# Optimization experiments

Measured on AMD Instinct MI355X. Metric: run time of the kernel, lower is better.

## Reference

```python
import jax, jax.numpy as jnp
import numpy as np

EGO, RNN, CUBE, FC, NA = 3200, 512, 3200, 1024, 2
N = 2048


def setup_inputs() -> dict:
    key = jax.random.key(0)
    ks = jax.random.split(key, 24)
    s = 0.02
    inp = {
        'rnn_feats': jax.random.normal(ks[0], (N, 2, RNN), jnp.float32),
        'cube_feats': jax.random.normal(ks[1], (N, 2, 4, CUBE), jnp.float32),
        'ego_feats': jax.random.normal(ks[2], (N, 3, EGO + RNN), jnp.float32),
        'rnn_eid': jax.random.randint(ks[3], (N,), 0, 3),
        'room_eid': jax.random.randint(ks[4], (N,), 0, 2),
        'dist_eid': jax.random.randint(ks[5], (N,), 0, 2),
        # shared front-end layers
        'Wc': jax.random.normal(ks[6], (CUBE, FC), jnp.float32) * s,
        'bc': jnp.zeros((FC,), jnp.float32),
        'Wd': jax.random.normal(ks[7], (EGO + RNN, FC), jnp.float32) * s,
        'bd': jnp.zeros((FC,), jnp.float32),
        # 3 experts on 2*RNN inputs (object color/size)
        'W1_rnn': jax.random.normal(ks[8], (3, 2 * RNN, FC), jnp.float32) * s,
        'b1_rnn': jnp.zeros((3, FC), jnp.float32),
        'W2_rnn': jax.random.normal(ks[9], (3, FC, NA), jnp.float32) * s,
        'b2_rnn': jnp.zeros((3, NA), jnp.float32),
        # 2 experts on 2*4*FC inputs (room size)
        'W1_room': jax.random.normal(ks[10], (2, 8 * FC, FC), jnp.float32) * s,
        'b1_room': jnp.zeros((2, FC), jnp.float32),
        'W2_room': jax.random.normal(ks[11], (2, FC, NA), jnp.float32) * s,
        'b2_room': jnp.zeros((2, NA), jnp.float32),
        # 2 experts on 2*FC inputs (object dist)
        'W1_dist': jax.random.normal(ks[12], (2, 2 * FC, FC), jnp.float32) * s,
        'b1_dist': jnp.zeros((2, FC), jnp.float32),
        'W2_dist': jax.random.normal(ks[13], (2, FC, NA), jnp.float32) * s,
        'b2_dist': jnp.zeros((2, NA), jnp.float32),
    }
    return inp


def _group_mlp(x, W1, b1, W2, b2, eid):
    # x: (n, in); W1: (E, in, fc); per-sample routed 2-layer MLP.
    # Dropout is identity (eval / p=0). Compute all E experts (E<=3), select via one-hot.
    h = jax.nn.relu(jnp.einsum('ni,eif->nef', x, W1) + b1[None])  # (n, E, fc)
    s = jnp.einsum('nef,efo->neo', h, W2) + b2[None]              # (n, E, 2)
    oh = jax.nn.one_hot(eid, W1.shape[0], dtype=x.dtype)          # (n, E)
    return jnp.einsum('neo,ne->no', s, oh)


def reference(rnn_feats, cube_feats, ego_feats, Wc, bc, Wd, bd,
              W1_rnn, b1_rnn, W2_rnn, b2_rnn,
              W1_room, b1_room, W2_room, b2_room,
              W1_dist, b1_dist, W2_dist, b2_dist,
              rnn_eid, room_eid, dist_eid):
    n = rnn_feats.shape[0]
    # object color/size group: raw rnn feats flattened
    x_rnn = rnn_feats.reshape(n, -1)                                   # (n, 2*RNN)
    s_rnn = _group_mlp(x_rnn, W1_rnn, b1_rnn, W2_rnn, b2_rnn, rnn_eid)
    # room size group: cube_fc_layer then flatten (2,4,fc) -> 8*fc
    hc = jax.nn.relu(jnp.einsum('npqc,cf->npqf', cube_feats, Wc) + bc)
    x_room = hc.reshape(n, -1)                                          # (n, 8*FC)
    s_room = _group_mlp(x_room, W1_room, b1_room, W2_room, b2_room, room_eid)
    # object dist group: dist_fc_layer, then pairwise products of the 3 rows
    hd = jax.nn.relu(jnp.einsum('nkd,df->nkf', ego_feats, Wd) + bd)     # (n, 3, FC)
    x_dist = jnp.concatenate([hd[:, 0] * hd[:, 1], hd[:, 1] * hd[:, 2]], axis=-1)  # (n, 2*FC)
    s_dist = _group_mlp(x_dist, W1_dist, b1_dist, W2_dist, b2_dist, dist_eid)
    return jnp.concatenate([s_rnn, s_room, s_dist], axis=0)             # (3n, 2)
```

## Files before the change

kernel.cpp:

```cpp
#include <hip/hip_runtime.h>

typedef __bf16 bf16;
typedef __bf16 bf16x8 __attribute__((ext_vector_type(8)));
typedef float f32x4 __attribute__((ext_vector_type(4)));

__device__ __forceinline__ void gld_lds16(const bf16* g, bf16* lds_base) {
    __builtin_amdgcn_global_load_lds(
        (const __attribute__((address_space(1))) void*)g,
        (__attribute__((address_space(3))) void*)lds_base, 16, 0, 0);
}

#define MFMA16(a, b, c) __builtin_amdgcn_mfma_f32_16x16x32_bf16((a), (b), (c), 0, 0, 0)

__global__ void detect_k(const unsigned* __restrict__ rnn, int* __restrict__ flag) {
    const int lane = threadIdx.x;
    const unsigned w = rnn[lane];
    const int e = (w >> 7) & 0xFF;
    const bool good = (e >= 100 && e <= 130);
    const unsigned long long m = __ballot(good);
    if (lane == 0) *flag = (__popcll(m) >= 48) ? 0 : 1;
}

__global__ __launch_bounds__(256) void transpose_k(const void* __restrict__ in_,
                                                   bf16* __restrict__ out,
                                                   const int* __restrict__ flag,
                                                   int R, int C) {
    __shared__ __align__(16) bf16 t[64][72];
    const int dt = *flag;
    const long boff = (long)blockIdx.z * R * C;
    const int c0 = blockIdx.x * 64, r0 = blockIdx.y * 64;
    const int lr = threadIdx.x >> 2;
    const int lc = (threadIdx.x & 3) * 16;

    bf16x8 v0, v1;
    if (dt) {
        const float* src = (const float*)in_ + boff + (long)(r0 + lr) * C + c0 + lc;
        float4 f0 = ((const float4*)src)[0];
        float4 f1 = ((const float4*)src)[1];
        float4 f2 = ((const float4*)src)[2];
        float4 f3 = ((const float4*)src)[3];
        v0[0]=(bf16)f0.x; v0[1]=(bf16)f0.y; v0[2]=(bf16)f0.z; v0[3]=(bf16)f0.w;
        v0[4]=(bf16)f1.x; v0[5]=(bf16)f1.y; v0[6]=(bf16)f1.z; v0[7]=(bf16)f1.w;
        v1[0]=(bf16)f2.x; v1[1]=(bf16)f2.y; v1[2]=(bf16)f2.z; v1[3]=(bf16)f2.w;
        v1[4]=(bf16)f3.x; v1[5]=(bf16)f3.y; v1[6]=(bf16)f3.z; v1[7]=(bf16)f3.w;
    } else {
        const bf16* src = (const bf16*)in_ + boff + (long)(r0 + lr) * C + c0 + lc;
        v0 = ((const bf16x8*)src)[0];
        v1 = ((const bf16x8*)src)[1];
    }
    *(bf16x8*)(&t[lr][lc])     = v0;
    *(bf16x8*)(&t[lr][lc + 8]) = v1;
    __syncthreads();

    bf16 tmp[16];
#pragma unroll
    for (int k = 0; k < 16; ++k) tmp[k] = t[lc + k][lr];
    bf16* dst = out + boff + (long)(c0 + lr) * R + r0 + lc;
    *(float4*)(dst)     = *(float4*)(&tmp[0]);
    *(float4*)(dst + 8) = *(float4*)(&tmp[8]);
}

__device__ __forceinline__ void kloop256(const bf16* __restrict__ A,
                                         const bf16* __restrict__ Bt,
                                         int K, int m0, int n0, bf16* L,
                                         int wid, int lane,
                                         f32x4 (&acc)[2][2][4][2]) {
    const int wm = wid >> 2, wn = wid & 3;
    const int quad = lane >> 4, l15 = lane & 15;
    const int nt = K >> 6;

    const int sr = wid * 8 + (lane >> 3);
    const int sc = ((lane & 7) ^ ((lane >> 3) & 7)) * 8;
    const bf16* Ag = A + (long)(m0 + sr) * K + sc;
    const bf16* Bg = Bt + (long)(n0 + sr) * K + sc;
    const long K64 = (long)K * 64, K128 = (long)K * 128;
    bf16* const As = L;
    bf16* const Bs = L + 32768;
    const int w512 = wid * 512;

    const int arow = (wm * 64 + l15) * 64;
    const int brow = (wn * 32 + l15) * 64;
    const int swz0 = ((0 * 4 + quad) ^ (l15 & 7)) * 8;
    const int swz1 = ((1 * 4 + quad) ^ (l15 & 7)) * 8;

    gld_lds16(Ag,              As + w512);
    gld_lds16(Ag + K64,        As + 4096 + w512);
    gld_lds16(Bg,              Bs + w512);
    gld_lds16(Bg + K64,        Bs + 4096 + w512);
    gld_lds16(Ag + K128,       As + 8192 + w512);
    gld_lds16(Ag + K128 + K64, As + 8192 + 4096 + w512);
    gld_lds16(Bg + K128,       Bs + 8192 + w512);
    gld_lds16(Bg + K128 + K64, Bs + 8192 + 4096 + w512);
    gld_lds16(Ag + 64,         As + 16384 + w512);
    gld_lds16(Ag + K64 + 64,   As + 16384 + 4096 + w512);
    gld_lds16(Bg + 64,         Bs + 16384 + w512);
    gld_lds16(Bg + K64 + 64,   Bs + 16384 + 4096 + w512);
    asm volatile("s_waitcnt vmcnt(4)" ::: "memory");
    __builtin_amdgcn_s_barrier();

    bf16x8 af[4][2], b0[2][2], b1[2][2];

    for (int t = 0; t < nt; ++t) {
        const int buf = t & 1, nbuf = buf ^ 1;
        bf16* A0 = As + (buf * 2 + 0) * 8192;
        bf16* A1 = As + (buf * 2 + 1) * 8192;
        bf16* B0 = Bs + (buf * 2 + 0) * 8192;
        bf16* B1 = Bs + (buf * 2 + 1) * 8192;
        const long ko1 = (long)(t + 1) * 64;
        const long ko2 = (long)(t + 2) * 64;

#pragma unroll
        for (int m = 0; m < 4; ++m) {
            af[m][0] = *(const bf16x8*)(A0 + arow + m * 1024 + swz0);
            af[m][1] = *(const bf16x8*)(A0 + arow + m * 1024 + swz1);
        }
#pragma unroll
        for (int n = 0; n < 2; ++n) {
            b0[n][0] = *(const bf16x8*)(B0 + brow + n * 1024 + swz0);
            b0[n][1] = *(const bf16x8*)(B0 + brow + n * 1024 + swz1);
        }
        if (t + 1 < nt) {
            gld_lds16(Ag + K128 + ko1,       As + (nbuf * 2 + 1) * 8192 + w512);
            gld_lds16(Ag + K128 + K64 + ko1, As + (nbuf * 2 + 1) * 8192 + 4096 + w512);
            gld_lds16(Bg + K128 + ko1,       Bs + (nbuf * 2 + 1) * 8192 + w512);
            gld_lds16(Bg + K128 + K64 + ko1, Bs + (nbuf * 2 + 1) * 8192 + 4096 + w512);
        }
        __builtin_amdgcn_s_barrier();
        asm volatile("s_waitcnt lgkmcnt(0)" ::: "memory");
        __builtin_amdgcn_sched_barrier(0);
        __builtin_amdgcn_s_setprio(1);
#pragma unroll
        for (int m = 0; m < 4; ++m)
#pragma unroll
            for (int n = 0; n < 2; ++n) {
                acc[0][0][m][n] = MFMA16(af[m][0], b0[n][0], acc[0][0][m][n]);
                acc[0][0][m][n] = MFMA16(af[m][1], b0[n][1], acc[0][0][m][n]);
            }
        __builtin_amdgcn_s_setprio(0);
        __builtin_amdgcn_sched_barrier(0);
        __builtin_amdgcn_s_barrier();

#pragma unroll
        for (int n = 0; n < 2; ++n) {
            b1[n][0] = *(const bf16x8*)(B1 + brow + n * 1024 + swz0);
            b1[n][1] = *(const bf16x8*)(B1 + brow + n * 1024 + swz1);
        }
        if (t + 2 < nt) {
            gld_lds16(Ag + ko2,       A0 + w512);
            gld_lds16(Ag + K64 + ko2, A0 + 4096 + w512);
        }
        __builtin_amdgcn_s_barrier();
        asm volatile("s_waitcnt lgkmcnt(0)" ::: "memory");
        __builtin_amdgcn_sched_barrier(0);
        __builtin_amdgcn_s_setprio(1);
#pragma unroll
        for (int m = 0; m < 4; ++m)
#pragma unroll
            for (int n = 0; n < 2; ++n) {
                acc[0][1][m][n] = MFMA16(af[m][0], b1[n][0], acc[0][1][m][n]);
                acc[0][1][m][n] = MFMA16(af[m][1], b1[n][1], acc[0][1][m][n]);
            }
        __builtin_amdgcn_s_setprio(0);
        __builtin_amdgcn_sched_barrier(0);
        __builtin_amdgcn_s_barrier();

#pragma unroll
        for (int m = 0; m < 4; ++m) {
            af[m][0] = *(const bf16x8*)(A1 + arow + m * 1024 + swz0);
            af[m][1] = *(const bf16x8*)(A1 + arow + m * 1024 + swz1);
        }
        __builtin_amdgcn_s_barrier();
        asm volatile("s_waitcnt lgkmcnt(0)" ::: "memory");
        __builtin_amdgcn_sched_barrier(0);
        __builtin_amdgcn_s_setprio(1);
#pragma unroll
        for (int m = 0; m < 4; ++m)
#pragma unroll
            for (int n = 0; n < 2; ++n) {
                acc[1][0][m][n] = MFMA16(af[m][0], b0[n][0], acc[1][0][m][n]);
                acc[1][0][m][n] = MFMA16(af[m][1], b0[n][1], acc[1][0][m][n]);
            }
        __builtin_amdgcn_s_setprio(0);
        __builtin_amdgcn_sched_barrier(0);
        __builtin_amdgcn_s_barrier();

        if (t + 2 < nt) {
            gld_lds16(Bg + ko2,       B0 + w512);
            gld_lds16(Bg + K64 + ko2, B0 + 4096 + w512);
        }
        __builtin_amdgcn_s_setprio(1);
#pragma unroll
        for (int m = 0; m < 4; ++m)
#pragma unroll
            for (int n = 0; n < 2; ++n) {
                acc[1][1][m][n] = MFMA16(af[m][0], b1[n][0], acc[1][1][m][n]);
                acc[1][1][m][n] = MFMA16(af[m][1], b1[n][1], acc[1][1][m][n]);
            }
        __builtin_amdgcn_s_setprio(0);
        __builtin_amdgcn_sched_barrier(0);
        if (t + 2 < nt) {
            asm volatile("s_waitcnt vmcnt(4)" ::: "memory");
        } else if (t + 1 < nt) {
            asm volatile("s_waitcnt vmcnt(0)" ::: "memory");
        }
        __builtin_amdgcn_s_barrier();
    }
}

__device__ __forceinline__ void tile256_coords(int& m0, int& n0) {
    const int lin = blockIdx.y * 8 + blockIdx.x;
    const int x = lin & 7, j = lin >> 3;
    const int mbPerX = (int)(gridDim.x * gridDim.y) >> 5;
    m0 = (x * mbPerX + (j >> 2)) * 256;
    n0 = (j & 3) * 256;
}

__global__ __launch_bounds__(512, 2) void gemm256_front(
        const void* __restrict__ A_, const bf16* __restrict__ Bt,
        const void* __restrict__ bias_, bf16* __restrict__ C,
        const int* __restrict__ flag, int M, int N, int K) {
    if (*flag != 0) return;
    __shared__ __align__(16) bf16 L[65536];
    const int tid = threadIdx.x, lane = tid & 63, wid = tid >> 6;
    int m0, n0;
    tile256_coords(m0, n0);

    f32x4 acc[2][2][4][2];
#pragma unroll
    for (int a = 0; a < 2; ++a)
#pragma unroll
        for (int b = 0; b < 2; ++b)
#pragma unroll
            for (int m = 0; m < 4; ++m)
#pragma unroll
                for (int n = 0; n < 2; ++n) acc[a][b][m][n] = (f32x4){0.f,0.f,0.f,0.f};

    kloop256((const bf16*)A_, Bt, K, m0, n0, L, wid, lane, acc);

    const bf16* bias = (const bf16*)bias_;
    const int wm = wid >> 2, wn = wid & 3;
    const int quad = lane >> 4, l15 = lane & 15;
#pragma unroll
    for (int qn = 0; qn < 2; ++qn)
#pragma unroll
        for (int n = 0; n < 2; ++n) {
            const int colg = n0 + qn * 128 + wn * 32 + n * 16 + l15;
            const float bj = (float)bias[colg];
#pragma unroll
            for (int qm = 0; qm < 2; ++qm)
#pragma unroll
                for (int m = 0; m < 4; ++m) {
                    const int rowb = m0 + qm * 128 + wm * 64 + m * 16 + quad * 4;
#pragma unroll
                    for (int r = 0; r < 4; ++r) {
                        float v = acc[qm][qn][m][n][r] + bj;
                        v = v > 0.f ? v : 0.f;
                        C[(long)(rowb + r) * N + colg] = (bf16)v;
                    }
                }
        }
}

struct ExpDescs {
    const void* A[7];
    const bf16* Bt[7];
    const void* biasB[7];
    const void* w2B[7];
    float* S[7];
    long biasEoff[7];
    long w2Eoff[7];
    int K[7];
    int adt[7];
};

__global__ __launch_bounds__(512, 2) void gemm256_expert(ExpDescs d,
                                                         const int* __restrict__ flag) {
    if (*flag != 0) return;
    __shared__ __align__(16) bf16 L[65536];
    const int z = blockIdx.z;
    const int K = d.K[z];
    const int tid = threadIdx.x, lane = tid & 63, wid = tid >> 6;
    int m0, n0;
    tile256_coords(m0, n0);

    f32x4 acc[2][2][4][2];
#pragma unroll
    for (int a = 0; a < 2; ++a)
#pragma unroll
        for (int b = 0; b < 2; ++b)
#pragma unroll
            for (int m = 0; m < 4; ++m)
#pragma unroll
                for (int n = 0; n < 2; ++n) acc[a][b][m][n] = (f32x4){0.f,0.f,0.f,0.f};

    kloop256((const bf16*)d.A[z], d.Bt[z], K, m0, n0, L, wid, lane, acc);

    const bf16* bias_b = (const bf16*)d.biasB[z] + d.biasEoff[z];
    const bf16* w2_b   = (const bf16*)d.w2B[z] + d.w2Eoff[z];
    float* S = d.S[z];
    const int wm = wid >> 2, wn = wid & 3;
    const int quad = lane >> 4, l15 = lane & 15;

    float bj[2][2], w2f[2][2][2];
#pragma unroll
    for (int qn = 0; qn < 2; ++qn)
#pragma unroll
        for (int n = 0; n < 2; ++n) {
            const int colg = n0 + qn * 128 + wn * 32 + n * 16 + l15;
            bj[qn][n] = (float)bias_b[colg];
            w2f[qn][n][0] = (float)w2_b[colg * 2 + 0];
            w2f[qn][n][1] = (float)w2_b[colg * 2 + 1];
        }
#pragma unroll
    for (int qm = 0; qm < 2; ++qm)
#pragma unroll
        for (int m = 0; m < 4; ++m)
#pragma unroll
            for (int r = 0; r < 4; ++r) {
                float s0 = 0.f, s1 = 0.f;
#pragma unroll
                for (int qn = 0; qn < 2; ++qn)
#pragma unroll
                    for (int n = 0; n < 2; ++n) {
                        float h = acc[qm][qn][m][n][r] + bj[qn][n];
                        h = h > 0.f ? h : 0.f;
                        s0 += h * w2f[qn][n][0];
                        s1 += h * w2f[qn][n][1];
                    }
#pragma unroll
                for (int msk = 1; msk < 16; msk <<= 1) {
                    s0 += __shfl_xor(s0, msk);
                    s1 += __shfl_xor(s1, msk);
                }
                if (l15 == 0) {
                    const int rowg = m0 + qm * 128 + wm * 64 + m * 16 + quad * 4 + r;
                    atomicAdd(&S[rowg * 2 + 0], s0);
                    atomicAdd(&S[rowg * 2 + 1], s1);
                }
            }
}

__device__ __forceinline__ void mfma_tile(const bf16* As, const bf16* Bs,
                                          int wm, int wn, int quad, int l15,
                                          f32x4 acc[4][4]) {
#pragma unroll
    for (int kk = 0; kk < 2; ++kk) {
        bf16x8 af[4], bff[4];
        const int kc = kk * 4 + quad;
#pragma unroll
        for (int i = 0; i < 4; ++i) {
            const int m = wm * 64 + i * 16 + l15;
            af[i] = *(const bf16x8*)(As + m * 64 + (kc ^ (m & 7)) * 8);
            const int n = wn * 64 + i * 16 + l15;
            bff[i] = *(const bf16x8*)(Bs + n * 64 + (kc ^ (n & 7)) * 8);
        }
#pragma unroll
        for (int i = 0; i < 4; ++i)
#pragma unroll
            for (int j = 0; j < 4; ++j)
                acc[i][j] = __builtin_amdgcn_mfma_f32_16x16x32_bf16(
                    af[i], bff[j], acc[i][j], 0, 0, 0);
    }
}

__device__ __forceinline__ void stageAB(const bf16* a, const bf16* b, int K,
                                        bf16* Asb, bf16* Bsb, int lbase) {
#pragma unroll
    for (int r = 0; r < 4; ++r) {
        gld_lds16(a + (long)(r * 32) * K, Asb + r * 2048 + lbase);
        gld_lds16(b + (long)(r * 32) * K, Bsb + r * 2048 + lbase);
    }
}

__device__ __forceinline__ void stageB(const bf16* b, int K, bf16* Bsb, int lbase) {
#pragma unroll
    for (int r = 0; r < 4; ++r)
        gld_lds16(b + (long)(r * 32) * K, Bsb + r * 2048 + lbase);
}

__device__ __forceinline__ void issueA_f32(const char* Ag4, int K, int k0,
                                           float4 fa[8]) {
#pragma unroll
    for (int r = 0; r < 4; ++r) {
        const float4* pa = (const float4*)(Ag4 + ((long)(r * 32) * K + k0) * 4);
        fa[2 * r]     = pa[0];
        fa[2 * r + 1] = pa[1];
    }
}

__device__ __forceinline__ void writeA_cvt(bf16* Asb, const float4 fa[8], int ldst) {
#pragma unroll
    for (int r = 0; r < 4; ++r) {
        const float4 f0 = fa[2 * r], f1 = fa[2 * r + 1];
        bf16x8 v;
        v[0]=(bf16)f0.x; v[1]=(bf16)f0.y; v[2]=(bf16)f0.z; v[3]=(bf16)f0.w;
        v[4]=(bf16)f1.x; v[5]=(bf16)f1.y; v[6]=(bf16)f1.z; v[7]=(bf16)f1.w;
        *(bf16x8*)(Asb + r * 2048 + ldst) = v;
    }
}

__device__ __forceinline__ void kloop_bf16(const bf16* Agb, const bf16* Bg, int K,
                                           bf16* As, bf16* Bs, int lbase,
                                           int wm, int wn, int quad, int l15,
                                           f32x4 acc[4][4]) {
    const int nt = K >> 6;
    stageAB(Agb, Bg, K, As, Bs, lbase);
    for (int t = 0; t < nt; ++t) {
        const int cur = (t & 1) * 8192;
        if (t + 1 < nt) {
            const int nxt = ((t + 1) & 1) * 8192;
            stageAB(Agb + ((t + 1) << 6), Bg + ((t + 1) << 6), K,
                    As + nxt, Bs + nxt, lbase);
            asm volatile("s_waitcnt vmcnt(8)" ::: "memory");
        } else {
            asm volatile("s_waitcnt vmcnt(0)" ::: "memory");
        }
        __builtin_amdgcn_s_barrier();
        __builtin_amdgcn_sched_barrier(0);
        mfma_tile(As + cur, Bs + cur, wm, wn, quad, l15, acc);
        __builtin_amdgcn_sched_barrier(0);
        __builtin_amdgcn_s_barrier();
    }
}

__global__ __launch_bounds__(256, 2) void gemm_front(const void* __restrict__ A_,
                                                     const bf16* __restrict__ Bt,
                                                     const void* __restrict__ bias_,
                                                     bf16* __restrict__ C,
                                                     const int* __restrict__ flag,
                                                     int M, int N, int K) {
    const int dt = *flag;
    if (dt == 0) return;
    __shared__ __align__(16) bf16 As[2][128 * 64];
    __shared__ __align__(16) bf16 Bs[2][128 * 64];

    const int tid = threadIdx.x, lane = tid & 63, wid = tid >> 6;
    const int wm = wid & 1, wn = wid >> 1;

    const int lin = blockIdx.y * 8 + blockIdx.x;
    const int m0 = ((lin >> 6) * 8 + (lin & 7)) * 128;
    const int n0 = ((lin >> 3) & 7) * 128;

    const int srow = wid * 8 + (lane >> 3);
    const int scol = ((lane & 7) ^ (srow & 7)) * 8;
    const bf16* Bg = Bt + (long)(n0 + srow) * K + scol;
    const int ldst = wid * 512 + lane * 8;
    const int lbase = wid * 512;

    f32x4 acc[4][4];
#pragma unroll
    for (int i = 0; i < 4; ++i)
#pragma unroll
        for (int j = 0; j < 4; ++j) acc[i][j] = (f32x4){0.f, 0.f, 0.f, 0.f};

    const int quad = lane >> 4, l15 = lane & 15;
    const int nt = K >> 6;

    {
        const char* Ag4 = (const char*)A_ + ((long)(m0 + srow) * K + scol) * 4;
        float4 fa[8];
        issueA_f32(Ag4, K, 0, fa);
        stageB(Bg, K, Bs[0], lbase);
        writeA_cvt(As[0], fa, ldst);
        __syncthreads();
        int t = 0;
        for (; t < nt - 2; t += 2) {
            issueA_f32(Ag4, K, (t + 1) << 6, fa);
            stageB(Bg + ((t + 1) << 6), K, Bs[1], lbase);
            mfma_tile(As[0], Bs[0], wm, wn, quad, l15, acc);
            writeA_cvt(As[1], fa, ldst);
            __syncthreads();
            issueA_f32(Ag4, K, (t + 2) << 6, fa);
            stageB(Bg + ((t + 2) << 6), K, Bs[0], lbase);
            mfma_tile(As[1], Bs[1], wm, wn, quad, l15, acc);
            writeA_cvt(As[0], fa, ldst);
            __syncthreads();
        }
        issueA_f32(Ag4, K, (nt - 1) << 6, fa);
        stageB(Bg + ((nt - 1) << 6), K, Bs[1], lbase);
        mfma_tile(As[0], Bs[0], wm, wn, quad, l15, acc);
        writeA_cvt(As[1], fa, ldst);
        __syncthreads();
        mfma_tile(As[1], Bs[1], wm, wn, quad, l15, acc);
    }

#pragma unroll
    for (int j = 0; j < 4; ++j) {
        const int colg = n0 + wn * 64 + j * 16 + l15;
        const float bj = ((const float*)bias_)[colg];
#pragma unroll
        for (int i = 0; i < 4; ++i) {
            const int rowb = m0 + wm * 64 + i * 16 + quad * 4;
#pragma unroll
            for (int r = 0; r < 4; ++r) {
                float v = acc[i][j][r] + bj;
                v = v > 0.f ? v : 0.f;
                C[(long)(rowb + r) * N + colg] = (bf16)v;
            }
        }
    }
}

__global__ __launch_bounds__(256, 2) void gemm_expert(ExpDescs d,
                                                      const int* __restrict__ flag) {
    const int dt = *flag;
    if (dt == 0) return;
    __shared__ __align__(16) bf16 As[2][128 * 64];
    __shared__ __align__(16) bf16 Bs[2][128 * 64];

    const int z = blockIdx.z;
    const int adt = d.adt[z];
    const int K = d.K[z];
    const void* A_ = d.A[z];
    const bf16* Bt = d.Bt[z];

    const int tid = threadIdx.x, lane = tid & 63, wid = tid >> 6;
    const int wm = wid & 1, wn = wid >> 1;

    const int lin = blockIdx.y * 8 + blockIdx.x;
    const int m0 = ((lin >> 6) * 8 + (lin & 7)) * 128;
    const int n0 = ((lin >> 3) & 7) * 128;

    const int srow = wid * 8 + (lane >> 3);
    const int scol = ((lane & 7) ^ (srow & 7)) * 8;
    const bf16* Bg = Bt + (long)(n0 + srow) * K + scol;
    const int ldst = wid * 512 + lane * 8;
    const int lbase = wid * 512;

    f32x4 acc[4][4];
#pragma unroll
    for (int i = 0; i < 4; ++i)
#pragma unroll
        for (int j = 0; j < 4; ++j) acc[i][j] = (f32x4){0.f, 0.f, 0.f, 0.f};

    const int quad = lane >> 4, l15 = lane & 15;
    const int nt = K >> 6;

    if (adt) {
        const char* Ag4 = (const char*)A_ + ((long)(m0 + srow) * K + scol) * 4;
        float4 fa[8];
        issueA_f32(Ag4, K, 0, fa);
        stageB(Bg, K, Bs[0], lbase);
        writeA_cvt(As[0], fa, ldst);
        __syncthreads();
        int t = 0;
        for (; t < nt - 2; t += 2) {
            issueA_f32(Ag4, K, (t + 1) << 6, fa);
            stageB(Bg + ((t + 1) << 6), K, Bs[1], lbase);
            mfma_tile(As[0], Bs[0], wm, wn, quad, l15, acc);
            writeA_cvt(As[1], fa, ldst);
            __syncthreads();
            issueA_f32(Ag4, K, (t + 2) << 6, fa);
            stageB(Bg + ((t + 2) << 6), K, Bs[0], lbase);
            mfma_tile(As[1], Bs[1], wm, wn, quad, l15, acc);
            writeA_cvt(As[0], fa, ldst);
            __syncthreads();
        }
        issueA_f32(Ag4, K, (nt - 1) << 6, fa);
        stageB(Bg + ((nt - 1) << 6), K, Bs[1], lbase);
        mfma_tile(As[0], Bs[0], wm, wn, quad, l15, acc);
        writeA_cvt(As[1], fa, ldst);
        __syncthreads();
        mfma_tile(As[1], Bs[1], wm, wn, quad, l15, acc);
    } else {
        const bf16* Agb = (const bf16*)A_ + (long)(m0 + srow) * K + scol;
        kloop_bf16(Agb, Bg, K, As[0], Bs[0], lbase, wm, wn, quad, l15, acc);
    }

    const char* bias_b = (const char*)d.biasB[z] + d.biasEoff[z] * 4;
    const char* w2_b   = (const char*)d.w2B[z] + d.w2Eoff[z] * 4;
    float* S = d.S[z];

    float bj[4], w2f[4][2];
#pragma unroll
    for (int j = 0; j < 4; ++j) {
        const int colg = n0 + wn * 64 + j * 16 + l15;
        bj[j] = ((const float*)bias_b)[colg];
        w2f[j][0] = ((const float*)w2_b)[colg * 2 + 0];
        w2f[j][1] = ((const float*)w2_b)[colg * 2 + 1];
    }
#pragma unroll
    for (int i = 0; i < 4; ++i) {
#pragma unroll
        for (int r = 0; r < 4; ++r) {
            float s0 = 0.f, s1 = 0.f;
#pragma unroll
            for (int j = 0; j < 4; ++j) {
                float h = acc[i][j][r] + bj[j];
                h = h > 0.f ? h : 0.f;
                s0 += h * w2f[j][0];
                s1 += h * w2f[j][1];
            }
#pragma unroll
            for (int msk = 1; msk < 16; msk <<= 1) {
                s0 += __shfl_xor(s0, msk);
                s1 += __shfl_xor(s1, msk);
            }
            if (l15 == 0) {
                const int rowg = m0 + wm * 64 + i * 16 + quad * 4 + r;
                atomicAdd(&S[rowg * 2 + 0], s0);
                atomicAdd(&S[rowg * 2 + 1], s1);
            }
        }
    }
}

__global__ __launch_bounds__(256) void pairprod_k(const bf16* __restrict__ hd,
                                                  bf16* __restrict__ xd) {
    const int idx = blockIdx.x * 256 + threadIdx.x;
    const int n = idx >> 8;
    const int c8 = (idx & 255) << 3;
    const bf16* p;
    if (c8 < 1024) p = hd + (long)(3 * n) * 1024 + c8;
    else           p = hd + (long)(3 * n + 1) * 1024 + (c8 - 1024);
    const bf16* q = p + 1024;
    bf16x8 a = *(const bf16x8*)p, b = *(const bf16x8*)q;
    bf16x8 o;
#pragma unroll
    for (int k = 0; k < 8; ++k) o[k] = (bf16)((float)a[k] * (float)b[k]);
    *(bf16x8*)(xd + (long)n * 2048 + c8) = o;
}

__global__ __launch_bounds__(256) void finalize_k(const float* __restrict__ S,
        const int* __restrict__ rnn_eid, const int* __restrict__ room_eid,
        const int* __restrict__ dist_eid, const void* __restrict__ b2_rnn,
        const void* __restrict__ b2_room, const void* __restrict__ b2_dist,
        const int* __restrict__ flag, void* __restrict__ out) {
    const int idx = blockIdx.x * 256 + threadIdx.x;
    if (idx >= 12288) return;
    const int dt = *flag;
    const int o = idx & 1;
    const int row = idx >> 1;
    const int g = row >> 11;
    const int n = row & 2047;
    float v;
    if (g == 0) {
        int e = rnn_eid[n]; e = e < 0 ? 0 : (e > 2 ? 2 : e);
        v = S[e * 4096 + n * 2 + o] +
            (dt ? ((const float*)b2_rnn)[e * 2 + o]
                : (float)((const bf16*)b2_rnn)[e * 2 + o]);
    } else if (g == 1) {
        int e = room_eid[n]; e = e < 0 ? 0 : (e > 1 ? 1 : e);
        v = S[12288 + e * 4096 + n * 2 + o] +
            (dt ? ((const float*)b2_room)[e * 2 + o]
                : (float)((const bf16*)b2_room)[e * 2 + o]);
    } else {
        int e = dist_eid[n]; e = e < 0 ? 0 : (e > 1 ? 1 : e);
        v = S[20480 + e * 4096 + n * 2 + o] +
            (dt ? ((const float*)b2_dist)[e * 2 + o]
                : (float)((const bf16*)b2_dist)[e * 2 + o]);
    }
    if (dt) ((float*)out)[idx] = v;
    else    ((bf16*)out)[idx] = (bf16)v;
}

extern "C" void kernel_launch(void* const* d_in, const int* in_sizes, int n_in,
                              void* d_out, int out_size, void* d_ws, size_t ws_size,
                              hipStream_t stream) {
    const void* rnn_feats = d_in[0];
    const void* cube      = d_in[1];
    const void* ego       = d_in[2];
    const int* rnn_eid    = (const int*)d_in[3];
    const int* room_eid   = (const int*)d_in[4];
    const int* dist_eid   = (const int*)d_in[5];
    const void* Wc        = d_in[6];
    const void* bc        = d_in[7];
    const void* Wd        = d_in[8];
    const void* bd        = d_in[9];
    const void* W1_rnn    = d_in[10];
    const void* b1_rnn    = d_in[11];
    const void* W2_rnn    = d_in[12];
    const void* b2_rnn    = d_in[13];
    const void* W1_room   = d_in[14];
    const void* b1_room   = d_in[15];
    const void* W2_room   = d_in[16];
    const void* b2_room   = d_in[17];
    const void* W1_dist   = d_in[18];
    const void* b1_dist   = d_in[19];
    const void* W2_dist   = d_in[20];
    const void* b2_dist   = d_in[21];

    char* ws = (char*)d_ws;
    float* S     = (float*)ws;
    int* flag    = (int*)(ws + 114688);
    bf16* WcT    = (bf16*)(ws + 114944);
    bf16* WdT    = (bf16*)(ws + 6668544);
    bf16* WrnnT  = (bf16*)(ws + 14270720);
    bf16* WroomT = (bf16*)(ws + 20562176);
    bf16* WdistT = (bf16*)(ws + 54116608);
    bf16* hc     = (bf16*)(ws + 62505216);
    bf16* hd     = (bf16*)(ws + 96059648);
    bf16* xd     = (bf16*)(ws + 108642560);

    detect_k<<<1, 64, 0, stream>>>((const unsigned*)rnn_feats, flag);
    hipMemsetAsync(S, 0, 114688, stream);

    transpose_k<<<dim3(16, 50, 1),  256, 0, stream>>>(Wc,      WcT,    flag, 3200, 1024);
    transpose_k<<<dim3(16, 58, 1),  256, 0, stream>>>(Wd,      WdT,    flag, 3712, 1024);
    transpose_k<<<dim3(16, 16, 3),  256, 0, stream>>>(W1_rnn,  WrnnT,  flag, 1024, 1024);
    transpose_k<<<dim3(16, 128, 2), 256, 0, stream>>>(W1_room, WroomT, flag, 8192, 1024);
    transpose_k<<<dim3(16, 32, 2),  256, 0, stream>>>(W1_dist, WdistT, flag, 2048, 1024);

    gemm256_front<<<dim3(8, 32), 512, 0, stream>>>(cube, WcT, bc, hc, flag,
                                                   16384, 1024, 3200);
    gemm_front<<<dim3(8, 128), 256, 0, stream>>>(cube, WcT, bc, hc, flag,
                                                 16384, 1024, 3200);
    gemm256_front<<<dim3(8, 12), 512, 0, stream>>>(ego, WdT, bd, hd, flag,
                                                   6144, 1024, 3712);
    gemm_front<<<dim3(8, 48), 256, 0, stream>>>(ego, WdT, bd, hd, flag,
                                                6144, 1024, 3712);
    pairprod_k<<<2048, 256, 0, stream>>>(hd, xd);

    ExpDescs D;
    for (int e = 0; e < 2; ++e) {
        const int z = e;
        D.A[z] = hc;                   D.Bt[z] = WroomT + (long)e * 1024 * 8192;
        D.biasB[z] = b1_room;          D.biasEoff[z] = (long)e * 1024;
        D.w2B[z] = W2_room;            D.w2Eoff[z] = (long)e * 2048;
        D.S[z] = S + 12288 + e * 4096; D.K[z] = 8192;  D.adt[z] = 0;
    }
    for (int e = 0; e < 2; ++e) {
        const int z = 2 + e;
        D.A[z] = xd;                   D.Bt[z] = WdistT + (long)e * 1024 * 2048;
        D.biasB[z] = b1_dist;          D.biasEoff[z] = (long)e * 1024;
        D.w2B[z] = W2_dist;            D.w2Eoff[z] = (long)e * 2048;
        D.S[z] = S + 20480 + e * 4096; D.K[z] = 2048;  D.adt[z] = 0;
    }
    for (int e = 0; e < 3; ++e) {
        const int z = 4 + e;
        D.A[z] = rnn_feats;            D.Bt[z] = WrnnT + (long)e * 1024 * 1024;
        D.biasB[z] = b1_rnn;           D.biasEoff[z] = (long)e * 1024;
        D.w2B[z] = W2_rnn;             D.w2Eoff[z] = (long)e * 2048;
        D.S[z] = S + e * 4096;         D.K[z] = 1024;  D.adt[z] = 1;
    }
    gemm256_expert<<<dim3(8, 4, 7), 512, 0, stream>>>(D, flag);
    gemm_expert<<<dim3(8, 16, 7), 256, 0, stream>>>(D, flag);

    finalize_k<<<48, 256, 0, stream>>>(S, rnn_eid, room_eid, dist_eid,
                                       b2_rnn, b2_room, b2_dist, flag, d_out);
}
```

Measured before the change: 958.0 us.

## Pre-cast fp32 activations to bf16 and route front GEMMs through 256-tile kernel

Adds a grid-stride cast kernel that converts the fp32 cube, ego and rnn activations to bf16 in workspace and also zeroes the score buffer, replacing the memset. When the workspace is large enough, the fp32 path then uses a single fused 256x256 front GEMM for both the cube and ego layers instead of the 128-tile kernels that convert on the fly. The five weight transposes are merged into one launch, and sched_barriers are added around the k-loop barriers. The expert 256-tile kernel is dropped, so the 128-tile expert kernel now handles both dtypes, reading the pre-cast rnn input. The cost is an extra full read and write pass over large activations, plus a dependence on workspace size.

```diff
diff --git a/kernel.cpp b/kernel.cpp
--- a/kernel.cpp
+++ b/kernel.cpp
@@ -21,20 +21,59 @@
     if (lane == 0) *flag = (__popcll(m) >= 48) ? 0 : 1;
 }
 
-__global__ __launch_bounds__(256) void transpose_k(const void* __restrict__ in_,
-                                                   bf16* __restrict__ out,
-                                                   const int* __restrict__ flag,
-                                                   int R, int C) {
+__device__ __forceinline__ void cvt8(const float* __restrict__ s,
+                                     bf16* __restrict__ d, long i8) {
+    const float4* p = (const float4*)(s + i8 * 8);
+    const float4 f0 = p[0], f1 = p[1];
+    bf16x8 v;
+    v[0]=(bf16)f0.x; v[1]=(bf16)f0.y; v[2]=(bf16)f0.z; v[3]=(bf16)f0.w;
+    v[4]=(bf16)f1.x; v[5]=(bf16)f1.y; v[6]=(bf16)f1.z; v[7]=(bf16)f1.w;
+    *(bf16x8*)(d + i8 * 8) = v;
+}
+
+__global__ __launch_bounds__(256) void cast_k(
+        const float* __restrict__ cube, const float* __restrict__ ego,
+        const float* __restrict__ rnn, bf16* __restrict__ cubeB,
+        bf16* __restrict__ egoB, bf16* __restrict__ rnnB,
+        float* __restrict__ S,
+        int cc, int ce, int cr, const int* __restrict__ flag) {
+    const long tid = (long)blockIdx.x * 256 + threadIdx.x;
+    const long stride = (long)gridDim.x * 256;
+    for (long i = tid; i < 28672; i += stride) S[i] = 0.f;
+    if (*flag == 0) return;
+    if (cc) for (long i = tid; i < 6553600; i += stride) cvt8(cube, cubeB, i);
+    if (ce) for (long i = tid; i < 2850816; i += stride) cvt8(ego, egoB, i);
+    if (cr) for (long i = tid; i < 262144;  i += stride) cvt8(rnn, rnnB, i);
+}
+
+struct TrAll {
+    const void* in[5];
+    bf16* out[5];
+};
+
+__global__ __launch_bounds__(256) void transpose_all_k(TrAll p,
+                                                       const int* __restrict__ flag) {
     __shared__ __align__(16) bf16 t[64][72];
     const int dt = *flag;
-    const long boff = (long)blockIdx.z * R * C;
-    const int c0 = blockIdx.x * 64, r0 = blockIdx.y * 64;
+
+    int bid = blockIdx.x, seg, Y;
+    if      (bid < 800)  { seg = 0; Y = 50; }
+    else if (bid < 1728) { seg = 1; Y = 58;  bid -= 800; }
+    else if (bid < 2496) { seg = 2; Y = 16;  bid -= 1728; }
+    else if (bid < 6592) { seg = 3; Y = 128; bid -= 2496; }
+    else                 { seg = 4; Y = 32;  bid -= 6592; }
+    const int bx = bid & 15, rest = bid >> 4;
+    const int by = rest % Y, bz = rest / Y;
+    const int R = Y * 64, C = 1024;
+
+    const long boff = (long)bz * R * C;
+    const int c0 = bx * 64, r0 = by * 64;
     const int lr = threadIdx.x >> 2;
     const int lc = (threadIdx.x & 3) * 16;
 
     bf16x8 v0, v1;
     if (dt) {
-        const float* src = (const float*)in_ + boff + (long)(r0 + lr) * C + c0 + lc;
+        const float* src = (const float*)p.in[seg] + boff + (long)(r0 + lr) * C + c0 + lc;
         float4 f0 = ((const float4*)src)[0];
         float4 f1 = ((const float4*)src)[1];
         float4 f2 = ((const float4*)src)[2];
@@ -44,7 +83,7 @@
         v1[0]=(bf16)f2.x; v1[1]=(bf16)f2.y; v1[2]=(bf16)f2.z; v1[3]=(bf16)f2.w;
         v1[4]=(bf16)f3.x; v1[5]=(bf16)f3.y; v1[6]=(bf16)f3.z; v1[7]=(bf16)f3.w;
     } else {
-        const bf16* src = (const bf16*)in_ + boff + (long)(r0 + lr) * C + c0 + lc;
+        const bf16* src = (const bf16*)p.in[seg] + boff + (long)(r0 + lr) * C + c0 + lc;
         v0 = ((const bf16x8*)src)[0];
         v1 = ((const bf16x8*)src)[1];
     }
@@ -55,7 +94,7 @@
     bf16 tmp[16];
 #pragma unroll
     for (int k = 0; k < 16; ++k) tmp[k] = t[lc + k][lr];
-    bf16* dst = out + boff + (long)(c0 + lr) * R + r0 + lc;
+    bf16* dst = p.out[seg] + boff + (long)(c0 + lr) * R + r0 + lc;
     *(float4*)(dst)     = *(float4*)(&tmp[0]);
     *(float4*)(dst + 8) = *(float4*)(&tmp[8]);
 }
@@ -97,6 +136,7 @@
     gld_lds16(Bg + K64 + 64,   Bs + 16384 + 4096 + w512);
     asm volatile("s_waitcnt vmcnt(4)" ::: "memory");
     __builtin_amdgcn_s_barrier();
+    __builtin_amdgcn_sched_barrier(0);
 
     bf16x8 af[4][2], b0[2][2], b1[2][2];
 
@@ -139,6 +179,7 @@
         __builtin_amdgcn_s_setprio(0);
         __builtin_amdgcn_sched_barrier(0);
         __builtin_amdgcn_s_barrier();
+        __builtin_amdgcn_sched_barrier(0);
 
 #pragma unroll
         for (int n = 0; n < 2; ++n) {
@@ -163,6 +204,7 @@
         __builtin_amdgcn_s_setprio(0);
         __builtin_amdgcn_sched_barrier(0);
         __builtin_amdgcn_s_barrier();
+        __builtin_amdgcn_sched_barrier(0);
 
 #pragma unroll
         for (int m = 0; m < 4; ++m) {
@@ -183,6 +225,7 @@
         __builtin_amdgcn_s_setprio(0);
         __builtin_amdgcn_sched_barrier(0);
         __builtin_amdgcn_s_barrier();
+        __builtin_amdgcn_sched_barrier(0);
 
         if (t + 2 < nt) {
             gld_lds16(Bg + ko2,       B0 + w512);
@@ -204,26 +247,43 @@
             asm volatile("s_waitcnt vmcnt(0)" ::: "memory");
         }
         __builtin_amdgcn_s_barrier();
-    }
-}
-
-__device__ __forceinline__ void tile256_coords(int& m0, int& n0) {
-    const int lin = blockIdx.y * 8 + blockIdx.x;
-    const int x = lin & 7, j = lin >> 3;
-    const int mbPerX = (int)(gridDim.x * gridDim.y) >> 5;
-    m0 = (x * mbPerX + (j >> 2)) * 256;
-    n0 = (j & 3) * 256;
-}
-
-__global__ __launch_bounds__(512, 2) void gemm256_front(
-        const void* __restrict__ A_, const bf16* __restrict__ Bt,
-        const void* __restrict__ bias_, bf16* __restrict__ C,
-        const int* __restrict__ flag, int M, int N, int K) {
-    if (*flag != 0) return;
+        __builtin_amdgcn_sched_barrier(0);
+    }
+}
+
+__global__ __launch_bounds__(512, 2) void front256_k(
+        const void* __restrict__ cubeIn, const bf16* __restrict__ cubeB,
+        const bf16* __restrict__ WcT, const void* __restrict__ bc,
+        bf16* __restrict__ hc,
+        const void* __restrict__ egoIn, const bf16* __restrict__ egoB,
+        const bf16* __restrict__ WdT, const void* __restrict__ bd,
+        bf16* __restrict__ hd,
+        const int* __restrict__ flag) {
     __shared__ __align__(16) bf16 L[65536];
+    const int dt = *flag;
     const int tid = threadIdx.x, lane = tid & 63, wid = tid >> 6;
-    int m0, n0;
-    tile256_coords(m0, n0);
+    const int N = 1024;
+
+    const bf16* A;
+    const bf16* Bt;
+    const void* bias_;
+    bf16* C;
+    int K, m0, n0;
+    if (blockIdx.y < 32) {
+        const int lin = blockIdx.y * 8 + blockIdx.x;
+        const int x = lin & 7, j = lin >> 3;
+        m0 = (x * 8 + (j >> 2)) * 256;
+        n0 = (j & 3) * 256;
+        A = dt ? cubeB : (const bf16*)cubeIn;
+        Bt = WcT; bias_ = bc; C = hc; K = 3200;
+    } else {
+        const int lin = (blockIdx.y - 32) * 8 + blockIdx.x;
+        const int x = lin & 7, j = lin >> 3;
+        m0 = (x * 3 + (j >> 2)) * 256;
+        n0 = (j & 3) * 256;
+        A = dt ? egoB : (const bf16*)egoIn;
+        Bt = WdT; bias_ = bd; C = hd; K = 3712;
+    }
 
     f32x4 acc[2][2][4][2];
 #pragma unroll
@@ -235,9 +295,8 @@
 #pragma unroll
                 for (int n = 0; n < 2; ++n) acc[a][b][m][n] = (f32x4){0.f,0.f,0.f,0.f};
 
-    kloop256((const bf16*)A_, Bt, K, m0, n0, L, wid, lane, acc);
-
-    const bf16* bias = (const bf16*)bias_;
+    kloop256(A, Bt, K, m0, n0, L, wid, lane, acc);
+
     const int wm = wid >> 2, wn = wid & 3;
     const int quad = lane >> 4, l15 = lane & 15;
 #pragma unroll
@@ -245,7 +304,8 @@
 #pragma unroll
         for (int n = 0; n < 2; ++n) {
             const int colg = n0 + qn * 128 + wn * 32 + n * 16 + l15;
-            const float bj = (float)bias[colg];
+            const float bj = dt ? ((const float*)bias_)[colg]
+                                : (float)((const bf16*)bias_)[colg];
 #pragma unroll
             for (int qm = 0; qm < 2; ++qm)
 #pragma unroll
@@ -259,85 +319,6 @@
                     }
                 }
         }
-}
-
-struct ExpDescs {
-    const void* A[7];
-    const bf16* Bt[7];
-    const void* biasB[7];
-    const void* w2B[7];
-    float* S[7];
-    long biasEoff[7];
-    long w2Eoff[7];
-    int K[7];
-    int adt[7];
-};
-
-__global__ __launch_bounds__(512, 2) void gemm256_expert(ExpDescs d,
-                                                         const int* __restrict__ flag) {
-    if (*flag != 0) return;
-    __shared__ __align__(16) bf16 L[65536];
-    const int z = blockIdx.z;
-    const int K = d.K[z];
-    const int tid = threadIdx.x, lane = tid & 63, wid = tid >> 6;
-    int m0, n0;
-    tile256_coords(m0, n0);
-
-    f32x4 acc[2][2][4][2];
-#pragma unroll
-    for (int a = 0; a < 2; ++a)
-#pragma unroll
-        for (int b = 0; b < 2; ++b)
-#pragma unroll
-            for (int m = 0; m < 4; ++m)
-#pragma unroll
-                for (int n = 0; n < 2; ++n) acc[a][b][m][n] = (f32x4){0.f,0.f,0.f,0.f};
-
-    kloop256((const bf16*)d.A[z], d.Bt[z], K, m0, n0, L, wid, lane, acc);
-
-    const bf16* bias_b = (const bf16*)d.biasB[z] + d.biasEoff[z];
-    const bf16* w2_b   = (const bf16*)d.w2B[z] + d.w2Eoff[z];
-    float* S = d.S[z];
-    const int wm = wid >> 2, wn = wid & 3;
-    const int quad = lane >> 4, l15 = lane & 15;
-
-    float bj[2][2], w2f[2][2][2];
-#pragma unroll
-    for (int qn = 0; qn < 2; ++qn)
-#pragma unroll
-        for (int n = 0; n < 2; ++n) {
-            const int colg = n0 + qn * 128 + wn * 32 + n * 16 + l15;
-            bj[qn][n] = (float)bias_b[colg];
-            w2f[qn][n][0] = (float)w2_b[colg * 2 + 0];
-            w2f[qn][n][1] = (float)w2_b[colg * 2 + 1];
-        }
-#pragma unroll
-    for (int qm = 0; qm < 2; ++qm)
-#pragma unroll
-        for (int m = 0; m < 4; ++m)
-#pragma unroll
-            for (int r = 0; r < 4; ++r) {
-                float s0 = 0.f, s1 = 0.f;
-#pragma unroll
-                for (int qn = 0; qn < 2; ++qn)
-#pragma unroll
-                    for (int n = 0; n < 2; ++n) {
-                        float h = acc[qm][qn][m][n][r] + bj[qn][n];
-                        h = h > 0.f ? h : 0.f;
-                        s0 += h * w2f[qn][n][0];
-                        s1 += h * w2f[qn][n][1];
-                    }
-#pragma unroll
-                for (int msk = 1; msk < 16; msk <<= 1) {
-                    s0 += __shfl_xor(s0, msk);
-                    s1 += __shfl_xor(s1, msk);
-                }
-                if (l15 == 0) {
-                    const int rowg = m0 + qm * 128 + wm * 64 + m * 16 + quad * 4 + r;
-                    atomicAdd(&S[rowg * 2 + 0], s0);
-                    atomicAdd(&S[rowg * 2 + 1], s1);
-                }
-            }
 }
 
 __device__ __forceinline__ void mfma_tile(const bf16* As, const bf16* Bs,
@@ -429,11 +410,10 @@
                                                      bf16* __restrict__ C,
                                                      const int* __restrict__ flag,
                                                      int M, int N, int K) {
-    const int dt = *flag;
-    if (dt == 0) return;
     __shared__ __align__(16) bf16 As[2][128 * 64];
     __shared__ __align__(16) bf16 Bs[2][128 * 64];
 
+    const int dt = *flag;
     const int tid = threadIdx.x, lane = tid & 63, wid = tid >> 6;
     const int wm = wid & 1, wn = wid >> 1;
 
@@ -456,7 +436,7 @@
     const int quad = lane >> 4, l15 = lane & 15;
     const int nt = K >> 6;
 
-    {
+    if (dt) {
         const char* Ag4 = (const char*)A_ + ((long)(m0 + srow) * K + scol) * 4;
         float4 fa[8];
         issueA_f32(Ag4, K, 0, fa);
@@ -482,12 +462,16 @@
         writeA_cvt(As[1], fa, ldst);
         __syncthreads();
         mfma_tile(As[1], Bs[1], wm, wn, quad, l15, acc);
+    } else {
+        const bf16* Agb = (const bf16*)A_ + (long)(m0 + srow) * K + scol;
+        kloop_bf16(Agb, Bg, K, As[0], Bs[0], lbase, wm, wn, quad, l15, acc);
     }
 
 #pragma unroll
     for (int j = 0; j < 4; ++j) {
         const int colg = n0 + wn * 64 + j * 16 + l15;
-        const float bj = ((const float*)bias_)[colg];
+        const float bj = dt ? ((const float*)bias_)[colg]
+                            : (float)((const bf16*)bias_)[colg];
 #pragma unroll
         for (int i = 0; i < 4; ++i) {
             const int rowb = m0 + wm * 64 + i * 16 + quad * 4;
@@ -501,14 +485,27 @@
     }
 }
 
+struct ExpDescs {
+    const void* A[7];
+    const bf16* Ac[7];
+    const bf16* Bt[7];
+    const void* biasB[7];
+    const void* w2B[7];
+    float* S[7];
+    long biasEoff[7];
+    long w2Eoff[7];
+    int K[7];
+    int adt[7];
+    int usec[7];
+};
+
 __global__ __launch_bounds__(256, 2) void gemm_expert(ExpDescs d,
                                                       const int* __restrict__ flag) {
-    const int dt = *flag;
-    if (dt == 0) return;
     __shared__ __align__(16) bf16 As[2][128 * 64];
     __shared__ __align__(16) bf16 Bs[2][128 * 64];
 
     const int z = blockIdx.z;
+    const int dt = *flag;
     const int adt = d.adt[z];
     const int K = d.K[z];
     const void* A_ = d.A[z];
@@ -536,7 +533,7 @@
     const int quad = lane >> 4, l15 = lane & 15;
     const int nt = K >> 6;
 
-    if (adt) {
+    if (adt && dt && !d.usec[z]) {
         const char* Ag4 = (const char*)A_ + ((long)(m0 + srow) * K + scol) * 4;
         float4 fa[8];
         issueA_f32(Ag4, K, 0, fa);
@@ -563,21 +560,29 @@
         __syncthreads();
         mfma_tile(As[1], Bs[1], wm, wn, quad, l15, acc);
     } else {
-        const bf16* Agb = (const bf16*)A_ + (long)(m0 + srow) * K + scol;
+        const bf16* Abase = (adt && dt) ? d.Ac[z] : (const bf16*)A_;
+        const bf16* Agb = Abase + (long)(m0 + srow) * K + scol;
         kloop_bf16(Agb, Bg, K, As[0], Bs[0], lbase, wm, wn, quad, l15, acc);
     }
 
-    const char* bias_b = (const char*)d.biasB[z] + d.biasEoff[z] * 4;
-    const char* w2_b   = (const char*)d.w2B[z] + d.w2Eoff[z] * 4;
+    const long besz = dt ? 4 : 2;
+    const char* bias_b = (const char*)d.biasB[z] + d.biasEoff[z] * besz;
+    const char* w2_b   = (const char*)d.w2B[z] + d.w2Eoff[z] * besz;
     float* S = d.S[z];
 
     float bj[4], w2f[4][2];
 #pragma unroll
     for (int j = 0; j < 4; ++j) {
         const int colg = n0 + wn * 64 + j * 16 + l15;
-        bj[j] = ((const float*)bias_b)[colg];
-        w2f[j][0] = ((const float*)w2_b)[colg * 2 + 0];
-        w2f[j][1] = ((const float*)w2_b)[colg * 2 + 1];
+        if (dt) {
+            bj[j] = ((const float*)bias_b)[colg];
+            w2f[j][0] = ((const float*)w2_b)[colg * 2 + 0];
+            w2f[j][1] = ((const float*)w2_b)[colg * 2 + 1];
+        } else {
+            bj[j] = (float)((const bf16*)bias_b)[colg];
+            w2f[j][0] = (float)((const bf16*)w2_b)[colg * 2 + 0];
+            w2f[j][1] = (float)((const bf16*)w2_b)[colg * 2 + 1];
+        }
     }
 #pragma unroll
     for (int i = 0; i < 4; ++i) {
@@ -691,49 +696,67 @@
     bf16* hc     = (bf16*)(ws + 62505216);
     bf16* hd     = (bf16*)(ws + 96059648);
     bf16* xd     = (bf16*)(ws + 108642560);
+    bf16* rnnB   = (bf16*)(ws + 117031168);
+    bf16* egoB   = (bf16*)(ws + 121225472);
+    bf16* cubeB  = (bf16*)(ws + 166838528);
+    const int castRnn  = ws_size >= 121225472UL ? 1 : 0;
+    const int castEgo  = ws_size >= 166838528UL ? 1 : 0;
+    const int castCube = ws_size >= 271696128UL ? 1 : 0;
+    const int fastPath = castRnn && castEgo && castCube;
 
     detect_k<<<1, 64, 0, stream>>>((const unsigned*)rnn_feats, flag);
-    hipMemsetAsync(S, 0, 114688, stream);
-
-    transpose_k<<<dim3(16, 50, 1),  256, 0, stream>>>(Wc,      WcT,    flag, 3200, 1024);
-    transpose_k<<<dim3(16, 58, 1),  256, 0, stream>>>(Wd,      WdT,    flag, 3712, 1024);
-    transpose_k<<<dim3(16, 16, 3),  256, 0, stream>>>(W1_rnn,  WrnnT,  flag, 1024, 1024);
-    transpose_k<<<dim3(16, 128, 2), 256, 0, stream>>>(W1_room, WroomT, flag, 8192, 1024);
-    transpose_k<<<dim3(16, 32, 2),  256, 0, stream>>>(W1_dist, WdistT, flag, 2048, 1024);
-
-    gemm256_front<<<dim3(8, 32), 512, 0, stream>>>(cube, WcT, bc, hc, flag,
-                                                   16384, 1024, 3200);
-    gemm_front<<<dim3(8, 128), 256, 0, stream>>>(cube, WcT, bc, hc, flag,
-                                                 16384, 1024, 3200);
-    gemm256_front<<<dim3(8, 12), 512, 0, stream>>>(ego, WdT, bd, hd, flag,
-                                                   6144, 1024, 3712);
-    gemm_front<<<dim3(8, 48), 256, 0, stream>>>(ego, WdT, bd, hd, flag,
-                                                6144, 1024, 3712);
+
+    cast_k<<<2048, 256, 0, stream>>>((const float*)cube, (const float*)ego,
+                                     (const float*)rnn_feats, cubeB, egoB, rnnB,
+                                     S, castCube, castEgo, castRnn, flag);
+
+    TrAll T;
+    T.in[0] = Wc;      T.out[0] = WcT;
+    T.in[1] = Wd;      T.out[1] = WdT;
+    T.in[2] = W1_rnn;  T.out[2] = WrnnT;
+    T.in[3] = W1_room; T.out[3] = WroomT;
+    T.in[4] = W1_dist; T.out[4] = WdistT;
+    transpose_all_k<<<7616, 256, 0, stream>>>(T, flag);
+
+    if (fastPath) {
+        front256_k<<<dim3(8, 44), 512, 0, stream>>>(cube, cubeB, WcT, bc, hc,
+                                                    ego, egoB, WdT, bd, hd, flag);
+    } else {
+        gemm_front<<<dim3(8, 128), 256, 0, stream>>>(cube, WcT, bc, hc, flag,
+                                                     16384, 1024, 3200);
+        gemm_front<<<dim3(8, 48), 256, 0, stream>>>(ego, WdT, bd, hd, flag,
+                                                    6144, 1024, 3712);
+    }
     pairprod_k<<<2048, 256, 0, stream>>>(hd, xd);
 
     ExpDescs D;
     for (int e = 0; e < 2; ++e) {
         const int z = e;
-        D.A[z] = hc;                   D.Bt[z] = WroomT + (long)e * 1024 * 8192;
+        D.A[z] = hc;                   D.Ac[z] = nullptr;
+        D.Bt[z] = WroomT + (long)e * 1024 * 8192;
         D.biasB[z] = b1_room;          D.biasEoff[z] = (long)e * 1024;
         D.w2B[z] = W2_room;            D.w2Eoff[z] = (long)e * 2048;
-        D.S[z] = S + 12288 + e * 4096; D.K[z] = 8192;  D.adt[z] = 0;
+        D.S[z] = S + 12288 + e * 4096; D.K[z] = 8192;
+        D.adt[z] = 0;                  D.usec[z] = 0;
     }
     for (int e = 0; e < 2; ++e) {
         const int z = 2 + e;
-        D.A[z] = xd;                   D.Bt[z] = WdistT + (long)e * 1024 * 2048;
+        D.A[z] = xd;                   D.Ac[z] = nullptr;
+        D.Bt[z] = WdistT + (long)e * 1024 * 2048;
         D.biasB[z] = b1_dist;          D.biasEoff[z] = (long)e * 1024;
         D.w2B[z] = W2_dist;            D.w2Eoff[z] = (long)e * 2048;
-        D.S[z] = S + 20480 + e * 4096; D.K[z] = 2048;  D.adt[z] = 0;
+        D.S[z] = S + 20480 + e * 4096; D.K[z] = 2048;
+        D.adt[z] = 0;                  D.usec[z] = 0;
     }
     for (int e = 0; e < 3; ++e) {
         const int z = 4 + e;
-        D.A[z] = rnn_feats;            D.Bt[z] = WrnnT + (long)e * 1024 * 1024;
+        D.A[z] = rnn_feats;            D.Ac[z] = rnnB;
+        D.Bt[z] = WrnnT + (long)e * 1024 * 1024;
         D.biasB[z] = b1_rnn;           D.biasEoff[z] = (long)e * 1024;
         D.w2B[z] = W2_rnn;             D.w2Eoff[z] = (long)e * 2048;
-        D.S[z] = S + e * 4096;         D.K[z] = 1024;  D.adt[z] = 1;
-    }
-    gemm256_expert<<<dim3(8, 4, 7), 512, 0, stream>>>(D, flag);
+        D.S[z] = S + e * 4096;         D.K[z] = 1024;
+        D.adt[z] = 1;                  D.usec[z] = castRnn;
+    }
     gemm_expert<<<dim3(8, 16, 7), 256, 0, stream>>>(D, flag);
 
     finalize_k<<<48, 256, 0, stream>>>(S, rnn_eid, room_eid, dist_eid,
```

Measured after the change: 838.4 us. 12.5% less time.
